# Performance work log

Hardware: AMD Instinct MI355X
Metric: run time of the kernel (lower is better)

The kernel has to match this reference:

```python
import jax, jax.numpy as jnp
import numpy as np

N_RAYS = 131072
N_PTS = 128
FAR = 1e10  # sentinel delta for the last sample, as in the torch code


def setup_inputs() -> dict:
    key = jax.random.key(0)
    k1, k2, k3 = jax.random.split(key, 3)
    # nonnegative densities (sigma)
    density = jax.random.uniform(k1, (N_RAYS, N_PTS), dtype=jnp.float32) * 2.0
    # per-sample RGB features
    feature = jax.random.uniform(k2, (N_RAYS, N_PTS, 3), dtype=jnp.float32)
    # monotonically increasing sample depths along each ray (near=0.1, far=6.1)
    depth_values = jnp.sort(
        jax.random.uniform(k3, (N_RAYS, N_PTS), dtype=jnp.float32) * 6.0 + 0.1,
        axis=-1,
    )
    return {"density": density, "feature": feature, "depth_values": depth_values}


def reference(density, feature, depth_values):
    # deltas: successive depth differences, huge value for the final sample  [N, P]
    deltas = jnp.concatenate(
        [depth_values[:, 1:] - depth_values[:, :-1],
         jnp.full_like(depth_values[:, :1], FAR)],
        axis=-1,
    )
    # per-sample transmittance factor t = exp(-sigma * delta)  [N, P]
    t = jnp.exp(-density * deltas)
    # exclusive cumulative transmittance T_i = prod_{j<i} t_j  (T_0 = 1)  [N, P]
    T = jnp.concatenate(
        [jnp.ones_like(t[:, :1]), jnp.cumprod(t, axis=1)[:, :-1]], axis=1
    )
    # alpha-compositing weights and RGB aggregation
    weights = T * (1.0 - t)                                  # [N, P]
    feat = jnp.sum(weights[..., None] * feature, axis=1)     # [N, 3]

    # depth estimate: torch code sets T>=1 entries to -inf, then selects T != -inf,
    # i.e. keeps samples where T < 1; normalizes t over selected samples.
    select = T < 1.0                                         # [N, P] bool
    t_sel = jnp.where(select, t, 0.0)
    denom = jnp.sum(t_sel, axis=1, keepdims=True)            # [N, 1]
    t_norm = t_sel / denom                                   # [N, P]
    depth = jnp.sum(t_norm * depth_values, axis=1)           # [N]
    depth = jnp.where(depth == 0.0, jnp.inf, depth)
    return feat, depth
```

## Files before the change

### kernel.cpp

```cpp
#include <hip/hip_runtime.h>
#include <math.h>

#define N_RAYS 131072
#define N_PTS  128
#define FAR_DELTA 1e10f

template<int CTRL>
__device__ __forceinline__ float dpp_mov(float src, float old) {
    return __builtin_bit_cast(float, __builtin_amdgcn_update_dpp(
        __builtin_bit_cast(int, old), __builtin_bit_cast(int, src),
        CTRL, 0xF, 0xF, false));
}

__global__ __launch_bounds__(256, 4) void volrender_kernel(
    const float* __restrict__ density,
    const float* __restrict__ feature,
    const float* __restrict__ depthv,
    float* __restrict__ out)
{
    const int tid = threadIdx.x;
    const int sub = tid & 15;
    const int ray = blockIdx.x * 16 + (tid >> 4);

    const size_t sbase = (size_t)ray * N_PTS + sub * 8;

    const float4 d0 = *reinterpret_cast<const float4*>(depthv + sbase);
    const float4 d1 = *reinterpret_cast<const float4*>(depthv + sbase + 4);
    const float4 g0 = *reinterpret_cast<const float4*>(density + sbase);
    const float4 g1 = *reinterpret_cast<const float4*>(density + sbase + 4);

    const float* fb = feature + (size_t)ray * (N_PTS * 3) + sub * 24;
    float ff[24];
    #pragma unroll
    for (int k = 0; k < 6; ++k)
        *reinterpret_cast<float4*>(&ff[4 * k]) =
            *reinterpret_cast<const float4*>(fb + 4 * k);

    const float dv[8] = {d0.x, d0.y, d0.z, d0.w, d1.x, d1.y, d1.z, d1.w};
    const float sg[8] = {g0.x, g0.y, g0.z, g0.w, g1.x, g1.y, g1.z, g1.w};

    const float dn = dpp_mov<0x101>(d0.x, 0.0f);
    float dl[8];
    #pragma unroll
    for (int j = 0; j < 7; ++j) dl[j] = dv[j + 1] - dv[j];
    dl[7] = (sub == 15) ? FAR_DELTA : (dn - dv[7]);

    float t[8], p[8];
    #pragma unroll
    for (int j = 0; j < 8; ++j) t[j] = __expf(-sg[j] * dl[j]);
    p[0] = t[0];
    #pragma unroll
    for (int j = 1; j < 8; ++j) p[j] = p[j - 1] * t[j];

    float scan = p[7];
    scan *= dpp_mov<0x111>(scan, 1.0f);
    scan *= dpp_mov<0x112>(scan, 1.0f);
    scan *= dpp_mov<0x114>(scan, 1.0f);
    scan *= dpp_mov<0x118>(scan, 1.0f);
    const float excl = dpp_mov<0x111>(scan, 1.0f);

    float fx = 0.f, fy = 0.f, fz = 0.f, st = 0.f, sd = 0.f;
    #pragma unroll
    for (int j = 0; j < 8; ++j) {
        const float T = (j == 0) ? excl : excl * p[j - 1];
        const float w = fmaf(-T, t[j], T);
        fx = fmaf(w, ff[3 * j + 0], fx);
        fy = fmaf(w, ff[3 * j + 1], fy);
        fz = fmaf(w, ff[3 * j + 2], fz);
        const float ts = (T < 1.0f) ? t[j] : 0.0f;
        st += ts;
        sd = fmaf(ts, dv[j], sd);
    }

    #define RED16(x)                 \
        x += dpp_mov<0x108>(x, 0.f); \
        x += dpp_mov<0x104>(x, 0.f); \
        x += dpp_mov<0x102>(x, 0.f); \
        x += dpp_mov<0x101>(x, 0.f);
    RED16(fx) RED16(fy) RED16(fz) RED16(st) RED16(sd)
    #undef RED16

    if (sub == 0) {
        out[(size_t)ray * 3 + 0] = fx;
        out[(size_t)ray * 3 + 1] = fy;
        out[(size_t)ray * 3 + 2] = fz;
        const float dep = sd / st;
        out[(size_t)N_RAYS * 3 + ray] = (dep == 0.0f) ? INFINITY : dep;
    }
}

extern "C" void kernel_launch(void* const* d_in, const int* in_sizes, int n_in,
                              void* d_out, int out_size, void* d_ws, size_t ws_size,
                              hipStream_t stream) {
    const float* density = (const float*)d_in[0];
    const float* feature = (const float*)d_in[1];
    const float* depthv  = (const float*)d_in[2];
    float* out = (float*)d_out;

    const int grid = N_RAYS / 16;
    volrender_kernel<<<grid, 256, 0, stream>>>(density, feature, depthv, out);
}
```

Before: 66.68 us.

## Process four ray groups per block with double-buffered register tiles

```diff
diff --git a/kernel.cpp b/kernel.cpp
--- a/kernel.cpp
+++ b/kernel.cpp
@@ -12,34 +12,45 @@
         CTRL, 0xF, 0xF, false));
 }
 
-__global__ __launch_bounds__(256, 4) void volrender_kernel(
-    const float* __restrict__ density,
-    const float* __restrict__ feature,
-    const float* __restrict__ depthv,
-    float* __restrict__ out)
-{
-    const int tid = threadIdx.x;
-    const int sub = tid & 15;
-    const int ray = blockIdx.x * 16 + (tid >> 4);
+struct Tile {
+    float4 d0, d1, g0, g1;
+    float4 f0, f1, f2, f3, f4, f5;
+};
 
+__device__ __forceinline__ Tile load_tile(const float* __restrict__ density,
+                                          const float* __restrict__ feature,
+                                          const float* __restrict__ depthv,
+                                          int ray, int sub) {
+    Tile t;
     const size_t sbase = (size_t)ray * N_PTS + sub * 8;
+    t.d0 = *reinterpret_cast<const float4*>(depthv  + sbase);
+    t.d1 = *reinterpret_cast<const float4*>(depthv  + sbase + 4);
+    t.g0 = *reinterpret_cast<const float4*>(density + sbase);
+    t.g1 = *reinterpret_cast<const float4*>(density + sbase + 4);
+    const float* fb = feature + (size_t)ray * (N_PTS * 3) + sub * 24;
+    t.f0 = *reinterpret_cast<const float4*>(fb +  0);
+    t.f1 = *reinterpret_cast<const float4*>(fb +  4);
+    t.f2 = *reinterpret_cast<const float4*>(fb +  8);
+    t.f3 = *reinterpret_cast<const float4*>(fb + 12);
+    t.f4 = *reinterpret_cast<const float4*>(fb + 16);
+    t.f5 = *reinterpret_cast<const float4*>(fb + 20);
+    return t;
+}
 
-    const float4 d0 = *reinterpret_cast<const float4*>(depthv + sbase);
-    const float4 d1 = *reinterpret_cast<const float4*>(depthv + sbase + 4);
-    const float4 g0 = *reinterpret_cast<const float4*>(density + sbase);
-    const float4 g1 = *reinterpret_cast<const float4*>(density + sbase + 4);
+__device__ __forceinline__ void compute_tile(const Tile& tl, int ray, int sub,
+                                             float* __restrict__ out) {
+    const float dv[8] = {tl.d0.x, tl.d0.y, tl.d0.z, tl.d0.w,
+                         tl.d1.x, tl.d1.y, tl.d1.z, tl.d1.w};
+    const float sg[8] = {tl.g0.x, tl.g0.y, tl.g0.z, tl.g0.w,
+                         tl.g1.x, tl.g1.y, tl.g1.z, tl.g1.w};
+    const float ff[24] = {tl.f0.x, tl.f0.y, tl.f0.z, tl.f0.w,
+                          tl.f1.x, tl.f1.y, tl.f1.z, tl.f1.w,
+                          tl.f2.x, tl.f2.y, tl.f2.z, tl.f2.w,
+                          tl.f3.x, tl.f3.y, tl.f3.z, tl.f3.w,
+                          tl.f4.x, tl.f4.y, tl.f4.z, tl.f4.w,
+                          tl.f5.x, tl.f5.y, tl.f5.z, tl.f5.w};
 
-    const float* fb = feature + (size_t)ray * (N_PTS * 3) + sub * 24;
-    float ff[24];
-    #pragma unroll
-    for (int k = 0; k < 6; ++k)
-        *reinterpret_cast<float4*>(&ff[4 * k]) =
-            *reinterpret_cast<const float4*>(fb + 4 * k);
-
-    const float dv[8] = {d0.x, d0.y, d0.z, d0.w, d1.x, d1.y, d1.z, d1.w};
-    const float sg[8] = {g0.x, g0.y, g0.z, g0.w, g1.x, g1.y, g1.z, g1.w};
-
-    const float dn = dpp_mov<0x101>(d0.x, 0.0f);
+    const float dn = dpp_mov<0x101>(dv[0], 0.0f);
     float dl[8];
     #pragma unroll
     for (int j = 0; j < 7; ++j) dl[j] = dv[j + 1] - dv[j];
@@ -89,6 +100,27 @@
     }
 }
 
+__global__ __launch_bounds__(256) void volrender_kernel(
+    const float* __restrict__ density,
+    const float* __restrict__ feature,
+    const float* __restrict__ depthv,
+    float* __restrict__ out)
+{
+    const int tid = threadIdx.x;
+    const int sub = tid & 15;
+    const int grp = tid >> 4;
+    const int rayBase = blockIdx.x * 64 + grp;
+
+    Tile A = load_tile(density, feature, depthv, rayBase +  0, sub);
+    Tile B = load_tile(density, feature, depthv, rayBase + 16, sub);
+    compute_tile(A, rayBase +  0, sub, out);
+    A = load_tile(density, feature, depthv, rayBase + 32, sub);
+    compute_tile(B, rayBase + 16, sub, out);
+    B = load_tile(density, feature, depthv, rayBase + 48, sub);
+    compute_tile(A, rayBase + 32, sub, out);
+    compute_tile(B, rayBase + 48, sub, out);
+}
+
 extern "C" void kernel_launch(void* const* d_in, const int* in_sizes, int n_in,
                               void* d_out, int out_size, void* d_ws, size_t ws_size,
                               hipStream_t stream) {
@@ -97,6 +129,6 @@
     const float* depthv  = (const float*)d_in[2];
     float* out = (float*)d_out;
 
-    const int grid = N_RAYS / 16;
+    const int grid = N_RAYS / 64;
     volrender_kernel<<<grid, 256, 0, stream>>>(density, feature, depthv, out);
 }
```

New measurement: 71.70 us. +7.5%, slower.
